# Kernel optimization log

Measured on AMD Instinct MI355X. Metric: run time of the kernel, lower is better.

## Reference

```python
import jax, jax.numpy as jnp
import numpy as np
from jax import lax

OBS_LEN = 8
PRED_LEN = 12
DIM = 128      # hidden_dim
EMB = 64       # embedding_dim
HEADS = 4
MODES = 5
SCENE = 32     # peds per scene
NPED = 8192    # total peds (256 scenes)


def _lin(key, out_d, in_d):
    kw, kb = jax.random.split(key)
    w = jax.random.normal(kw, (out_d, in_d), jnp.float32) / np.sqrt(in_d).astype(np.float32)
    b = jax.random.normal(kb, (out_d,), jnp.float32) * 0.01
    return w, b


def _stack(key, n, out_d, in_d):
    ws, bs = zip(*[_lin(k, out_d, in_d) for k in jax.random.split(key, n)])
    return jnp.stack(ws), jnp.stack(bs)


def setup_inputs() -> dict:
    key = jax.random.key(0)
    ks = jax.random.split(key, 24)
    inp = {}
    inp['obs_traj'] = jax.random.normal(ks[0], (OBS_LEN, NPED, 2), jnp.float32)
    inp['pe_w'], inp['pe_b'] = _lin(ks[1], EMB, 2)
    inp['lstm_wih'], inp['lstm_bih'] = _lin(ks[2], 4 * DIM, EMB)
    inp['lstm_whh'], inp['lstm_bhh'] = _lin(ks[3], 4 * DIM, DIM)
    inp['rp_w1'], inp['rp_b1'] = _lin(ks[4], DIM // 2, 2)
    inp['rp_w2'], inp['rp_b2'] = _lin(ks[5], DIM, DIM // 2)
    inp['wq'], inp['bq'] = _lin(ks[6], DIM, DIM)
    inp['wk'], inp['bk'] = _lin(ks[7], DIM, DIM)
    inp['wv'], inp['bv'] = _lin(ks[8], DIM, DIM)
    inp['wo'], inp['bo'] = _lin(ks[9], DIM, DIM)
    inp['op_w'], inp['op_b'] = _lin(ks[10], DIM, 2 * DIM)
    inp['mp_w1'], inp['mp_b1'] = _lin(ks[11], DIM, 2 * DIM)
    inp['mp_w2'], inp['mp_b2'] = _lin(ks[12], MODES, DIM)
    inp['td_w1'], inp['td_b1'] = _stack(ks[13], MODES, DIM, 2 * DIM)
    inp['td_w2'], inp['td_b2'] = _stack(ks[14], MODES, DIM, DIM)
    inp['td_w3'], inp['td_b3'] = _stack(ks[15], MODES, PRED_LEN * 2, DIM)
    inp['ud_w1'], inp['ud_b1'] = _stack(ks[16], MODES, DIM // 2, 2 * DIM)
    inp['ud_w2'], inp['ud_b2'] = _stack(ks[17], MODES, PRED_LEN * 2, DIM // 2)
    inp['scene_size'] = SCENE
    return inp


def reference(obs_traj, pe_w, pe_b, lstm_wih, lstm_bih, lstm_whh, lstm_bhh,
              rp_w1, rp_b1, rp_w2, rp_b2, wq, bq, wk, bk, wv, bv, wo, bo,
              op_w, op_b, mp_w1, mp_b1, mp_w2, mp_b2,
              td_w1, td_b1, td_w2, td_b2, td_w3, td_b3,
              ud_w1, ud_b1, ud_w2, ud_b2, scene_size):
    obs = jnp.transpose(obs_traj, (1, 0, 2))          # (N, T, 2)
    N = obs.shape[0]
    D = lstm_whh.shape[1]

    # ---- NodeHistoryEncoder: Linear embed + 1-layer LSTM, last hidden ----
    emb = jnp.einsum('ntd,ed->nte', obs, pe_w) + pe_b  # (N, T, EMB)

    def step(carry, x):
        h, c = carry
        g = x @ lstm_wih.T + lstm_bih + h @ lstm_whh.T + lstm_bhh
        i, f, gg, o = jnp.split(g, 4, axis=-1)          # torch gate order i,f,g,o
        c = jax.nn.sigmoid(f) * c + jax.nn.sigmoid(i) * jnp.tanh(gg)
        h = jax.nn.sigmoid(o) * jnp.tanh(c)
        return (h, c), None

    h0 = jnp.zeros((N, D), obs.dtype)
    (node_features, _), _ = lax.scan(step, (h0, h0), jnp.swapaxes(emb, 0, 1))
    last_pos = obs[:, -1, :]                            # (N, 2)

    # ---- EdgeEncoder: per-scene rel-pos-biased multi-head attention ----
    S = scene_size
    B = N // S
    feat = node_features.reshape(B, S, D)
    pos = last_pos.reshape(B, S, 2)
    rel = pos[:, None, :, :] - pos[:, :, None, :]       # [b,i,j] = pos_j - pos_i
    rel_enc = jax.nn.relu(jnp.einsum('bijd,hd->bijh', rel, rp_w1) + rp_b1)
    rel_enc = jnp.einsum('bijh,eh->bije', rel_enc, rp_w2) + rp_b2  # (B,S,S,D)
    kv = feat[:, None, :, :] + rel_enc                  # key == value
    dh = D // HEADS
    q = (feat @ wq.T + bq).reshape(B, S, HEADS, dh)
    kp = (jnp.einsum('bijd,ed->bije', kv, wk) + bk).reshape(B, S, S, HEADS, dh)
    vp = (jnp.einsum('bijd,ed->bije', kv, wv) + bv).reshape(B, S, S, HEADS, dh)
    scores = jnp.einsum('bihd,bijhd->bhij', q, kp) / np.sqrt(dh).astype(np.float32)
    attn = jax.nn.softmax(scores, axis=-1)
    ctx = jnp.einsum('bhij,bijhd->bihd', attn, vp).reshape(B, S, D)
    attn_out = ctx @ wo.T + bo
    edge = (jnp.concatenate([feat, attn_out], axis=-1) @ op_w.T + op_b).reshape(N, D)

    f_all = jnp.concatenate([node_features, edge], axis=-1)  # (N, 2D)

    # ---- GMMDecoder ----
    probs = jax.nn.softmax(jax.nn.relu(f_all @ mp_w1.T + mp_b1) @ mp_w2.T + mp_b2, axis=-1)
    h1 = jax.nn.relu(jnp.einsum('nd,mhd->nmh', f_all, td_w1) + td_b1)    # (N,M,D)
    h2 = jax.nn.relu(jnp.einsum('nmh,mgh->nmg', h1, td_w2) + td_b2)
    traj = (jnp.einsum('nmg,mog->nmo', h2, td_w3) + td_b3).reshape(N, MODES, PRED_LEN, 2)
    u1 = jax.nn.relu(jnp.einsum('nd,mhd->nmh', f_all, ud_w1) + ud_b1)
    sigmas = jax.nn.softplus(jnp.einsum('nmh,moh->nmo', u1, ud_w2) + ud_b2).reshape(N, MODES, PRED_LEN, 2)
    predictions = jnp.cumsum(traj, axis=2) + last_pos[:, None, None, :]
    return predictions, probs
```

## Files before the change

kernel.cpp:

```cpp
#include <hip/hip_runtime.h>
#include <math.h>

typedef __attribute__((ext_vector_type(8))) short short8;
typedef __attribute__((ext_vector_type(4))) float f32x4;

#define NPED 8192
#define INVS 0.1767766952966369f

#define B_WHH    0
#define B_WQKV   131072
#define B_WO     229376
#define B_OPW    262144
#define B_MPW1   327680
#define B_TDW1   393216
#define B_TDW2   720896
#define B_WK2PAD 884736
#define F_WIHE   950272
#define F_BEFF   954368
#define F_WV2T   956416
#define F_BQKV   989184
#define F_ZERO   990720
#define A_FEAT   991744
#define A_QKV    3088896
#define A_H1MP   9380352
#define A_H1TD   11477504
#define A_QW     11477504
#define B_TDW3C  21963264
#define F_TDB3C  22004224

__device__ __forceinline__ float bf2f(ushort u) {
  union { unsigned i; float f; } v; v.i = ((unsigned)u) << 16; return v.f;
}
__device__ __forceinline__ float blo(unsigned u) {
  union { unsigned i; float f; } v; v.i = u << 16; return v.f;
}
__device__ __forceinline__ float bhi(unsigned u) {
  union { unsigned i; float f; } v; v.i = u & 0xffff0000u; return v.f;
}
__device__ __forceinline__ ushort f2bf(float f) {
  union { float f; unsigned i; } v; v.f = f;
  unsigned r = v.i + 0x7fffu + ((v.i >> 16) & 1u);
  return (ushort)(r >> 16);
}

__global__ __launch_bounds__(256) void prep(
    const float* __restrict__ wih, const float* __restrict__ bih, const float* __restrict__ bhh,
    const float* __restrict__ pew, const float* __restrict__ peb,
    const float* __restrict__ wk, const float* __restrict__ wv,
    const float* __restrict__ rpw2, const float* __restrict__ rpb2,
    const float* __restrict__ bq, const float* __restrict__ bk, const float* __restrict__ bv,
    const float* __restrict__ whh, const float* __restrict__ wq, const float* __restrict__ wo,
    const float* __restrict__ opw, const float* __restrict__ mpw1,
    const float* __restrict__ tdw1, const float* __restrict__ tdw2,
    const float* __restrict__ tdw3, const float* __restrict__ tdb3,
    char* __restrict__ wsb) {
  int tid = blockIdx.x * 256 + threadIdx.x;
  float* wihe = (float*)(wsb + F_WIHE);
  float* beff = (float*)(wsb + F_BEFF);
  float* wv2T = (float*)(wsb + F_WV2T);
  float* bqkv = (float*)(wsb + F_BQKV);
  if (tid < 512) {
    int d = tid;
    float s0 = 0.f, s1 = 0.f, sb = 0.f;
    for (int e = 0; e < 64; ++e) {
      float w = wih[d * 64 + e];
      s0 += w * pew[e * 2]; s1 += w * pew[e * 2 + 1]; sb += w * peb[e];
    }
    wihe[d * 2] = s0; wihe[d * 2 + 1] = s1;
    beff[d] = bih[d] + bhh[d] + sb;
  } else if (tid < 33280) {
    int idx = tid - 512; int r = idx >> 7, d = idx & 127;
    int h = r >> 6, e = r & 63;
    float s = 0.f;
    if ((d >> 5) == h)
      for (int c = 0; c < 128; ++c) s += wk[d * 128 + c] * rpw2[c * 64 + e];
    ((ushort*)(wsb + B_WK2PAD))[idx] = f2bf(s);
  } else if (tid < 41472) {
    int idx = tid - 33280; int e = idx >> 7, hd = idx & 127;
    float s = 0.f;
    for (int c = 0; c < 128; ++c) s += wv[hd * 128 + c] * rpw2[c * 64 + e];
    wv2T[idx] = s;
  } else if (tid < 41600) {
    int d = tid - 41472;
    float s = bk[d];
    for (int c = 0; c < 128; ++c) s += wk[d * 128 + c] * rpb2[c];
    bqkv[128 + d] = s;
  } else if (tid < 41728) {
    int d = tid - 41600;
    float s = bv[d];
    for (int c = 0; c < 128; ++c) s += wv[d * 128 + c] * rpb2[c];
    bqkv[256 + d] = s;
  } else if (tid < 41856) {
    int d = tid - 41728;
    bqkv[d] = bq[d] * INVS;
  } else if (tid < 42112) {
    ((float*)(wsb + F_ZERO))[tid - 41856] = 0.f;
  } else {
    int i = tid - 42112;
    if (i < 65536) {
      ((ushort*)(wsb + B_WHH))[i] = f2bf(whh[i]);
    } else if (i < 114688) {
      int j = i - 65536; int n = j >> 7, k = j & 127;
      float v = (n < 128) ? wq[n * 128 + k] * INVS
                          : (n < 256) ? wk[(n - 128) * 128 + k] : wv[(n - 256) * 128 + k];
      ((ushort*)(wsb + B_WQKV))[j] = f2bf(v);
    } else if (i < 131072) {
      int j = i - 114688; ((ushort*)(wsb + B_WO))[j] = f2bf(wo[j]);
    } else if (i < 163840) {
      int j = i - 131072; ((ushort*)(wsb + B_OPW))[j] = f2bf(opw[j]);
    } else if (i < 196608) {
      int j = i - 163840; ((ushort*)(wsb + B_MPW1))[j] = f2bf(mpw1[j]);
    } else if (i < 360448) {
      int j = i - 196608; ((ushort*)(wsb + B_TDW1))[j] = f2bf(tdw1[j]);
    } else if (i < 442368) {
      int j = i - 360448; ((ushort*)(wsb + B_TDW2))[j] = f2bf(tdw2[j]);
    } else if (i < 462848) {
      int j = i - 442368; int m = j >> 12, r = j & 4095, o = r >> 7, k = r & 127;
      float s = 0.f;
      if (o < 24) {
        int c = o & 1, jj = o >> 1;
        for (int jp = 0; jp <= jj; ++jp) s += tdw3[(m * 24 + jp * 2 + c) * 128 + k];
      }
      ((ushort*)(wsb + B_TDW3C))[j] = f2bf(s);
    } else if (i < 462968) {
      int j = i - 462848; int m = j / 24, o = j % 24;
      int c = o & 1, jj = o >> 1;
      float s = 0.f;
      for (int jp = 0; jp <= jj; ++jp) s += tdb3[m * 24 + jp * 2 + c];
      ((float*)(wsb + F_TDB3C))[j] = s;
    }
  }
}

__global__ __launch_bounds__(512) void lstm_mfma(
    const float* __restrict__ obs, const ushort* __restrict__ whhb,
    const float* __restrict__ wihe, const float* __restrict__ beff,
    ushort* __restrict__ feat) {
  __shared__ ushort Hs[32 * 128];
  __shared__ float obs_s[8][32][2];
  int tid = threadIdx.x;
  int w = tid >> 6, l = tid & 63;
  int lm = l & 15, lg = l >> 4;
  int nb = blockIdx.x * 32;
  {
    int ts = tid >> 6, p = (tid >> 1) & 31, c = tid & 1;
    obs_s[ts][p][c] = obs[ts * (NPED * 2) + (nb + p) * 2 + c];
  }
  for (int i = tid; i < 4096; i += 512) Hs[i] = 0;
  short8 bfr[4][4];
  float wx0[4], wx1[4], be[4];
#pragma unroll
  for (int q = 0; q < 4; ++q) {
    int g = q * 128 + w * 16 + lm;
    wx0[q] = wihe[g * 2]; wx1[q] = wihe[g * 2 + 1]; be[q] = beff[g];
#pragma unroll
    for (int ks = 0; ks < 4; ++ks)
      bfr[q][ks] = *(const short8*)(const void*)&whhb[g * 128 + ks * 32 + lg * 8];
  }
  float cst[2][4] = {};
  __syncthreads();
  for (int ts = 0; ts < 8; ++ts) {
    f32x4 acc[2][4];
#pragma unroll
    for (int mi = 0; mi < 2; ++mi)
#pragma unroll
      for (int r = 0; r < 4; ++r) {
        int p = mi * 16 + lg * 4 + r;
        float ox = obs_s[ts][p][0], oy = obs_s[ts][p][1];
#pragma unroll
        for (int q = 0; q < 4; ++q)
          acc[mi][q][r] = be[q] + wx0[q] * ox + wx1[q] * oy;
      }
#pragma unroll
    for (int ks = 0; ks < 4; ++ks) {
      int p0 = lm, p1 = 16 + lm;
      short8 a0 = *(const short8*)(const void*)&Hs[p0 * 128 + ((ks * 32 + lg * 8) ^ ((p0 & 7) << 3))];
      short8 a1 = *(const short8*)(const void*)&Hs[p1 * 128 + ((ks * 32 + lg * 8) ^ ((p1 & 7) << 3))];
#pragma unroll
      for (int q = 0; q < 4; ++q) {
        acc[0][q] = __builtin_amdgcn_mfma_f32_16x16x32_bf16(a0, bfr[q][ks], acc[0][q], 0, 0, 0);
        acc[1][q] = __builtin_amdgcn_mfma_f32_16x16x32_bf16(a1, bfr[q][ks], acc[1][q], 0, 0, 0);
      }
    }
    __syncthreads();
    int d = w * 16 + lm;
#pragma unroll
    for (int mi = 0; mi < 2; ++mi)
#pragma unroll
      for (int r = 0; r < 4; ++r) {
        int p = mi * 16 + lg * 4 + r;
        float xi = acc[mi][0][r], xf = acc[mi][1][r], xg = acc[mi][2][r], xo = acc[mi][3][r];
        float ig = 1.f / (1.f + __expf(-xi));
        float fg = 1.f / (1.f + __expf(-xf));
        xg = fminf(fmaxf(xg, -30.f), 30.f);
        float eg = __expf(-2.f * xg);
        float gg = (1.f - eg) / (1.f + eg);
        float og = 1.f / (1.f + __expf(-xo));
        float cv = fg * cst[mi][r] + ig * gg;
        cst[mi][r] = cv;
        float cvc = fminf(fmaxf(cv, -30.f), 30.f);
        float ec = __expf(-2.f * cvc);
        float th = (1.f - ec) / (1.f + ec);
        ushort hb = f2bf(og * th);
        Hs[p * 128 + (d ^ ((p & 7) << 3))] = hb;
        if (ts == 7) feat[(size_t)(nb + p) * 128 + d] = hb;
      }
    __syncthreads();
  }
}

template<int NF>
__global__ __launch_bounds__(256) void mfma_gemm(
    const ushort* __restrict__ A1, int lda1, int K1,
    const ushort* __restrict__ A2, int lda2,
    const ushort* __restrict__ Bw, int K,
    const float* __restrict__ bias,
    ushort* __restrict__ out, int ldo, int ooff, int relu,
    int sB, int sBias, int sA1, int sOut) {
  int w = threadIdx.x >> 6, l = threadIdx.x & 63;
  int lm = l & 15, lg = l >> 4;
  int z = blockIdx.z;
  A1 += (size_t)z * sA1;
  Bw += (size_t)z * sB;
  bias += (size_t)z * sBias;
  out += (size_t)z * sOut;
  int row = blockIdx.x * 64 + w * 16 + lm;
  int col0 = blockIdx.y * (NF * 16);
  f32x4 acc[NF];
#pragma unroll
  for (int i = 0; i < NF; ++i) acc[i] = (f32x4){0.f, 0.f, 0.f, 0.f};
  const int nks = K >> 5;
  for (int ks = 0; ks < nks; ++ks) {
    int kb = ks * 32 + lg * 8;
    const ushort* ap = (ks * 32 < K1) ? (A1 + (size_t)row * lda1 + kb)
                                      : (A2 + (size_t)row * lda2 + (kb - K1));
    short8 af = *(const short8*)(const void*)ap;
#pragma unroll
    for (int ni = 0; ni < NF; ++ni) {
      short8 bf = *(const short8*)(const void*)(Bw + (size_t)(col0 + ni * 16 + lm) * K + kb);
      acc[ni] = __builtin_amdgcn_mfma_f32_16x16x32_bf16(af, bf, acc[ni], 0, 0, 0);
    }
  }
  int orow0 = blockIdx.x * 64 + w * 16 + lg * 4;
#pragma unroll
  for (int ni = 0; ni < NF; ++ni) {
    int c = col0 + ni * 16 + lm;
    float bv = bias[c];
#pragma unroll
    for (int r = 0; r < 4; ++r) {
      float v = acc[ni][r] + bv;
      if (relu) v = fmaxf(v, 0.f);
      out[(size_t)(orow0 + r) * ldo + ooff + c] = f2bf(v);
    }
  }
}

__global__ __launch_bounds__(256) void traj_mfma(
    const ushort* __restrict__ TD2, const ushort* __restrict__ w3c,
    const float* __restrict__ b3c, const float* __restrict__ obs,
    float* __restrict__ out) {
  int w = threadIdx.x >> 6, l = threadIdx.x & 63;
  int lm = l & 15, lg = l >> 4;
  int m = blockIdx.y;
  const ushort* A = TD2 + (size_t)m * (NPED * 128);
  const ushort* B = w3c + (size_t)m * 4096;
  int row = blockIdx.x * 64 + w * 16 + lm;
  f32x4 acc[2];
  acc[0] = (f32x4){0.f,0.f,0.f,0.f}; acc[1] = (f32x4){0.f,0.f,0.f,0.f};
#pragma unroll
  for (int ks = 0; ks < 4; ++ks) {
    int kb = ks * 32 + lg * 8;
    short8 af = *(const short8*)(const void*)(A + (size_t)row * 128 + kb);
#pragma unroll
    for (int ni = 0; ni < 2; ++ni) {
      short8 bf = *(const short8*)(const void*)(B + (ni * 16 + lm) * 128 + kb);
      acc[ni] = __builtin_amdgcn_mfma_f32_16x16x32_bf16(af, bf, acc[ni], 0, 0, 0);
    }
  }
  int orow0 = blockIdx.x * 64 + w * 16 + lg * 4;
#pragma unroll
  for (int ni = 0; ni < 2; ++ni) {
    int o = ni * 16 + lm;
    if (o < 24) {
      float bb = b3c[m * 24 + o];
      int c = o & 1;
#pragma unroll
      for (int r = 0; r < 4; ++r) {
        int n = orow0 + r;
        out[(size_t)n * 120 + m * 24 + o] = acc[ni][r] + bb + obs[7 * (NPED * 2) + n * 2 + c];
      }
    }
  }
}

__global__ __launch_bounds__(256) void attn_kernel(
    const float* __restrict__ obs, ushort* QKV, const ushort* __restrict__ QW,
    const float* __restrict__ wv2T,
    const float* __restrict__ rpw1, const float* __restrict__ rpb1) {
  __shared__ ushort K0s[32 * 128];
  __shared__ ushort V0s[32 * 128];
  __shared__ ushort renc[4 * 32 * 64];
  __shared__ float Qi[4][128];
  __shared__ float QWs[4][256];
  __shared__ float att[4][4][32];
  __shared__ float AR[4][4][64];
  __shared__ float rpx[64], rpy[64], rpb[64];
  __shared__ float posS[32][2];
  __shared__ float posI[4][2];
  int t = threadIdx.x;
  int scene = blockIdx.x & 255, ic = blockIdx.x >> 8;
  int i0 = ic * 4, sbase = scene * 32;

  for (int idx = t; idx < 1024; idx += 256) {
    int arr = idx >> 9, j = (idx >> 4) & 31, c = idx & 15;
    short8 v = *(const short8*)(const void*)&QKV[(size_t)(sbase + j) * 384 + 128 + arr * 128 + c * 8];
    ushort* dst = arr ? V0s : K0s;
    *(short8*)(void*)&dst[j * 128 + (c ^ (j & 7)) * 8] = v;
  }
  for (int idx = t; idx < 512; idx += 256) {
    int ii = idx >> 7, d = idx & 127;
    Qi[ii][d] = bf2f(QKV[(size_t)(sbase + i0 + ii) * 384 + d]);
  }
  for (int idx = t; idx < 1024; idx += 256) {
    int ii = idx >> 8, e = idx & 255;
    QWs[ii][e] = bf2f(QW[(size_t)(sbase + i0 + ii) * 256 + e]);
  }
  if (t < 64) posS[t >> 1][t & 1] = obs[7 * (NPED * 2) + (sbase + (t >> 1)) * 2 + (t & 1)];
  else if (t < 72) {
    int q = t - 64;
    posI[q >> 1][q & 1] = obs[7 * (NPED * 2) + (sbase + i0 + (q >> 1)) * 2 + (q & 1)];
  } else if (t >= 128 && t < 192) {
    int e = t - 128;
    rpx[e] = rpw1[e * 2]; rpy[e] = rpw1[e * 2 + 1]; rpb[e] = rpb1[e];
  }
  __syncthreads();

  for (int idx = t; idx < 1024; idx += 256) {
    int ii = idx >> 8, j = (idx >> 3) & 31, c = idx & 7;
    float dx = posS[j][0] - posI[ii][0], dy = posS[j][1] - posI[ii][1];
    short8 pk;
#pragma unroll
    for (int r = 0; r < 8; ++r) {
      int e = c * 8 + r;
      pk[r] = (short)f2bf(fmaxf(rpx[e] * dx + rpy[e] * dy + rpb[e], 0.f));
    }
    *(short8*)(void*)&renc[(ii * 32 + j) * 64 + (c ^ (j & 7)) * 8] = pk;
  }
  __syncthreads();

  for (int idx = t; idx < 512; idx += 256) {
    int ii = idx >> 7, h = (idx >> 5) & 3, j = idx & 31;
    float s = 0.f;
#pragma unroll
    for (int cc = 0; cc < 4; ++cc) {
      uint4 kv = *(const uint4*)(const void*)&K0s[j * 128 + (((h * 4 + cc) ^ (j & 7)) * 8)];
      const float4 qa = *(const float4*)&Qi[ii][h * 32 + cc * 8];
      const float4 qb = *(const float4*)&Qi[ii][h * 32 + cc * 8 + 4];
      s += blo(kv.x) * qa.x + bhi(kv.x) * qa.y + blo(kv.y) * qa.z + bhi(kv.y) * qa.w;
      s += blo(kv.z) * qb.x + bhi(kv.z) * qb.y + blo(kv.w) * qb.z + bhi(kv.w) * qb.w;
    }
#pragma unroll
    for (int c = 0; c < 8; ++c) {
      uint4 rv = *(const uint4*)(const void*)&renc[(ii * 32 + j) * 64 + ((c ^ (j & 7)) * 8)];
      const float4 wa = *(const float4*)&QWs[ii][c * 8];
      const float4 wb = *(const float4*)&QWs[ii][c * 8 + 4];
      (void)wa; (void)wb;
      const float4 ua = *(const float4*)&QWs[ii][h * 64 + c * 8];
      const float4 ub = *(const float4*)&QWs[ii][h * 64 + c * 8 + 4];
      s += blo(rv.x) * ua.x + bhi(rv.x) * ua.y + blo(rv.y) * ua.z + bhi(rv.y) * ua.w;
      s += blo(rv.z) * ub.x + bhi(rv.z) * ub.y + blo(rv.w) * ub.z + bhi(rv.w) * ub.w;
    }
    att[ii][h][j] = s;
  }
  __syncthreads();

  {
    int r = t >> 4, lj = t & 15;
    float v0 = att[r >> 2][r & 3][lj], v1 = att[r >> 2][r & 3][lj + 16];
    float mx = fmaxf(v0, v1);
    mx = fmaxf(mx, __shfl_xor(mx, 8, 16));
    mx = fmaxf(mx, __shfl_xor(mx, 4, 16));
    mx = fmaxf(mx, __shfl_xor(mx, 2, 16));
    mx = fmaxf(mx, __shfl_xor(mx, 1, 16));
    float e0 = expf(v0 - mx), e1 = expf(v1 - mx);
    float sm = e0 + e1;
    sm += __shfl_xor(sm, 8, 16);
    sm += __shfl_xor(sm, 4, 16);
    sm += __shfl_xor(sm, 2, 16);
    sm += __shfl_xor(sm, 1, 16);
    float inv = 1.f / sm;
    att[r >> 2][r & 3][lj] = e0 * inv;
    att[r >> 2][r & 3][lj + 16] = e1 * inv;
  }
  __syncthreads();

  {
    int ii = t >> 6, h = (t >> 4) & 3, e4 = t & 15;
    int c = e4 >> 1, off = (e4 & 1) * 4;
    float a0 = 0.f, a1 = 0.f, a2 = 0.f, a3 = 0.f;
    for (int j = 0; j < 32; ++j) {
      float av = att[ii][h][j];
      uint2 rv = *(const uint2*)(const void*)&renc[(ii * 32 + j) * 64 + ((c ^ (j & 7)) * 8) + off];
      a0 += av * blo(rv.x); a1 += av * bhi(rv.x);
      a2 += av * blo(rv.y); a3 += av * bhi(rv.y);
    }
    *(float4*)&AR[ii][h][e4 * 4] = make_float4(a0, a1, a2, a3);
  }
  __syncthreads();

  {
    int ii = t >> 6, l = t & 63;
    int h5 = l >> 5, hd4 = l & 31;
    int hd = hd4 * 4, h = hd >> 5;
    float c0 = 0.f, c1 = 0.f, c2 = 0.f, c3 = 0.f;
    int cch = hd >> 3, offh = hd & 7;
    for (int j = h5 * 16; j < h5 * 16 + 16; ++j) {
      float av = att[ii][h][j];
      uint2 vv = *(const uint2*)(const void*)&V0s[j * 128 + ((cch ^ (j & 7)) * 8) + offh];
      c0 += av * blo(vv.x); c1 += av * bhi(vv.x);
      c2 += av * blo(vv.y); c3 += av * bhi(vv.y);
    }
    for (int e4 = h5 * 8; e4 < h5 * 8 + 8; ++e4) {
      const float4 ar = *(const float4*)&AR[ii][h][e4 * 4];
#pragma unroll
      for (int r = 0; r < 4; ++r) {
        const float4 wv = *(const float4*)&wv2T[(e4 * 4 + r) * 128 + hd];
        float a = (r == 0) ? ar.x : (r == 1) ? ar.y : (r == 2) ? ar.z : ar.w;
        c0 += a * wv.x; c1 += a * wv.y; c2 += a * wv.z; c3 += a * wv.w;
      }
    }
    c0 += __shfl_xor(c0, 32); c1 += __shfl_xor(c1, 32);
    c2 += __shfl_xor(c2, 32); c3 += __shfl_xor(c3, 32);
    if (h5 == 0) {
      ushort4 o;
      o.x = f2bf(c0); o.y = f2bf(c1); o.z = f2bf(c2); o.w = f2bf(c3);
      *(ushort4*)(void*)&QKV[(size_t)(sbase + i0 + ii) * 384 + hd] = o;
    }
  }
}

__global__ __launch_bounds__(256) void probs_kernel(
    const ushort* __restrict__ H1, const float* __restrict__ mpw2,
    const float* __restrict__ mpb2, float* __restrict__ out) {
  __shared__ float Hsm[64][129];
  __shared__ float lgt[64][5];
  int t = threadIdx.x, nb = blockIdx.x * 64;
  for (int idx = t; idx < 8192; idx += 256) Hsm[idx >> 7][idx & 127] = bf2f(H1[(size_t)nb * 128 + idx]);
  __syncthreads();
  for (int idx = t; idx < 320; idx += 256) {
    int p = idx / 5, m = idx % 5;
    float s = mpb2[m];
    for (int k = 0; k < 128; ++k) s += Hsm[p][k] * mpw2[m * 128 + k];
    lgt[p][m] = s;
  }
  __syncthreads();
  if (t < 64) {
    float m0 = lgt[t][0];
#pragma unroll
    for (int j = 1; j < 5; ++j) m0 = fmaxf(m0, lgt[t][j]);
    float e[5], s = 0.f;
#pragma unroll
    for (int j = 0; j < 5; ++j) { e[j] = expf(lgt[t][j] - m0); s += e[j]; }
    float inv = 1.f / s;
#pragma unroll
    for (int j = 0; j < 5; ++j) out[983040 + (size_t)(nb + t) * 5 + j] = e[j] * inv;
  }
}

extern "C" void kernel_launch(void* const* d_in, const int* in_sizes, int n_in,
                              void* d_out, int out_size, void* d_ws, size_t ws_size,
                              hipStream_t stream) {
  (void)in_sizes; (void)n_in; (void)out_size; (void)ws_size;
  const float* obs  = (const float*)d_in[0];
  const float* pew  = (const float*)d_in[1];
  const float* peb  = (const float*)d_in[2];
  const float* wih  = (const float*)d_in[3];
  const float* bih  = (const float*)d_in[4];
  const float* whh  = (const float*)d_in[5];
  const float* bhh  = (const float*)d_in[6];
  const float* rpw1 = (const float*)d_in[7];
  const float* rpb1 = (const float*)d_in[8];
  const float* rpw2 = (const float*)d_in[9];
  const float* rpb2 = (const float*)d_in[10];
  const float* wq   = (const float*)d_in[11];
  const float* bq   = (const float*)d_in[12];
  const float* wk   = (const float*)d_in[13];
  const float* bk   = (const float*)d_in[14];
  const float* wv   = (const float*)d_in[15];
  const float* bv   = (const float*)d_in[16];
  const float* wo   = (const float*)d_in[17];
  const float* bo   = (const float*)d_in[18];
  const float* opw  = (const float*)d_in[19];
  const float* opb  = (const float*)d_in[20];
  const float* mpw1 = (const float*)d_in[21];
  const float* mpb1 = (const float*)d_in[22];
  const float* mpw2 = (const float*)d_in[23];
  const float* mpb2 = (const float*)d_in[24];
  const float* tdw1 = (const float*)d_in[25];
  const float* tdb1 = (const float*)d_in[26];
  const float* tdw2 = (const float*)d_in[27];
  const float* tdb2 = (const float*)d_in[28];
  const float* tdw3 = (const float*)d_in[29];
  const float* tdb3 = (const float*)d_in[30];
  char* wsb = (char*)d_ws;
  float* out = (float*)d_out;

  ushort* whhb   = (ushort*)(wsb + B_WHH);
  ushort* wqkvb  = (ushort*)(wsb + B_WQKV);
  ushort* wob    = (ushort*)(wsb + B_WO);
  ushort* opwb   = (ushort*)(wsb + B_OPW);
  ushort* mpw1b  = (ushort*)(wsb + B_MPW1);
  ushort* tdw1b  = (ushort*)(wsb + B_TDW1);
  ushort* tdw2b  = (ushort*)(wsb + B_TDW2);
  ushort* wk2pb  = (ushort*)(wsb + B_WK2PAD);
  ushort* tdw3cb = (ushort*)(wsb + B_TDW3C);
  ushort* featb  = (ushort*)(wsb + A_FEAT);
  ushort* qkvb   = (ushort*)(wsb + A_QKV);
  ushort* qwb    = (ushort*)(wsb + A_QW);
  ushort* h1mpb  = (ushort*)(wsb + A_H1MP);
  ushort* h1tdb  = (ushort*)(wsb + A_H1TD);

  prep<<<1973, 256, 0, stream>>>(wih, bih, bhh, pew, peb, wk, wv, rpw2, rpb2,
                                 bq, bk, bv, whh, wq, wo, opw, mpw1, tdw1, tdw2,
                                 tdw3, tdb3, wsb);
  lstm_mfma<<<256, 512, 0, stream>>>(obs, whhb, (float*)(wsb + F_WIHE),
                                     (float*)(wsb + F_BEFF), featb);
  mfma_gemm<4><<<dim3(128, 6, 1), 256, 0, stream>>>(
      featb, 128, 128, featb, 128, wqkvb, 128, (float*)(wsb + F_BQKV),
      qkvb, 384, 0, 0, 0, 0, 0, 0);
  mfma_gemm<4><<<dim3(128, 4, 1), 256, 0, stream>>>(
      qkvb, 384, 128, qkvb, 384, wk2pb, 128, (float*)(wsb + F_ZERO),
      qwb, 256, 0, 0, 0, 0, 0, 0);
  attn_kernel<<<2048, 256, 0, stream>>>(obs, qkvb, qwb, (float*)(wsb + F_WV2T), rpw1, rpb1);
  mfma_gemm<4><<<dim3(128, 2, 1), 256, 0, stream>>>(
      qkvb, 384, 128, qkvb, 384, wob, 128, bo, qkvb, 384, 128, 0, 0, 0, 0, 0);
  mfma_gemm<4><<<dim3(128, 2, 1), 256, 0, stream>>>(
      featb, 128, 128, qkvb + 128, 384, opwb, 256, opb, qkvb, 384, 256, 0, 0, 0, 0, 0);
  mfma_gemm<4><<<dim3(128, 2, 1), 256, 0, stream>>>(
      featb, 128, 128, qkvb + 256, 384, mpw1b, 256, mpb1, h1mpb, 128, 0, 1, 0, 0, 0, 0);
  probs_kernel<<<128, 256, 0, stream>>>(h1mpb, mpw2, mpb2, out);
  mfma_gemm<4><<<dim3(128, 2, 5), 256, 0, stream>>>(
      featb, 128, 128, qkvb + 256, 384, tdw1b, 256, tdb1, h1tdb, 128, 0, 1,
      32768, 128, 0, 1048576);
  mfma_gemm<8><<<dim3(128, 1, 5), 256, 0, stream>>>(
      h1tdb, 128, 128, h1tdb, 128, tdw2b, 128, tdb2, h1tdb, 128, 0, 1,
      16384, 128, 1048576, 1048576);
  traj_mfma<<<dim3(128, 5), 256, 0, stream>>>(h1tdb, tdw3cb, (float*)(wsb + F_TDB3C), obs, out);
}
```

Measured before the change: 297.3 us.

## Fold Wo into edge projection and fuse decoder MLP chains into single kernels

Folds the attention output projection (wo, bo) into the op_w edge projection in prep, so one GEMM replaces two. The mode-probability MLP and softmax become a single kernel, and the three trajectory-decoder layers are chained through shared memory in one kernel, so the h1/h2 intermediates no longer round-trip through global memory. The QKV buffer is widened to hold QW and edge outputs, and GEMM sizes become template constants so the k-loop fully unrolls. The trade-offs are heavier per-block register and LDS use, and lower parallelism in the fused decoder kernel.

```diff
diff --git a/kernel.cpp b/kernel.cpp
--- a/kernel.cpp
+++ b/kernel.cpp
@@ -9,24 +9,21 @@
 
 #define B_WHH    0
 #define B_WQKV   131072
-#define B_WO     229376
-#define B_OPW    262144
-#define B_MPW1   327680
-#define B_TDW1   393216
-#define B_TDW2   720896
-#define B_WK2PAD 884736
-#define F_WIHE   950272
-#define F_BEFF   954368
-#define F_WV2T   956416
-#define F_BQKV   989184
-#define F_ZERO   990720
-#define A_FEAT   991744
-#define A_QKV    3088896
-#define A_H1MP   9380352
-#define A_H1TD   11477504
-#define A_QW     11477504
-#define B_TDW3C  21963264
-#define F_TDB3C  22004224
+#define B_WK2PAD 229376
+#define B_OPWE   294912
+#define B_MPW1   360448
+#define B_TDW1   425984
+#define B_TDW2   753664
+#define B_TDW3C  917504
+#define F_WIHE   958464
+#define F_BEFF   962560
+#define F_WV2T   964608
+#define F_BQKV   997376
+#define F_BEDGE  998912
+#define F_TDB3C  999424
+#define F_ZERO   999936
+#define A_FEAT   1000960
+#define A_QKV    3098112
 
 __device__ __forceinline__ float bf2f(ushort u) {
   union { unsigned i; float f; } v; v.i = ((unsigned)u) << 16; return v.f;
@@ -50,15 +47,12 @@
     const float* __restrict__ rpw2, const float* __restrict__ rpb2,
     const float* __restrict__ bq, const float* __restrict__ bk, const float* __restrict__ bv,
     const float* __restrict__ whh, const float* __restrict__ wq, const float* __restrict__ wo,
-    const float* __restrict__ opw, const float* __restrict__ mpw1,
+    const float* __restrict__ opw, const float* __restrict__ opb, const float* __restrict__ bo,
+    const float* __restrict__ mpw1,
     const float* __restrict__ tdw1, const float* __restrict__ tdw2,
     const float* __restrict__ tdw3, const float* __restrict__ tdb3,
     char* __restrict__ wsb) {
   int tid = blockIdx.x * 256 + threadIdx.x;
-  float* wihe = (float*)(wsb + F_WIHE);
-  float* beff = (float*)(wsb + F_BEFF);
-  float* wv2T = (float*)(wsb + F_WV2T);
-  float* bqkv = (float*)(wsb + F_BQKV);
   if (tid < 512) {
     int d = tid;
     float s0 = 0.f, s1 = 0.f, sb = 0.f;
@@ -66,69 +60,77 @@
       float w = wih[d * 64 + e];
       s0 += w * pew[e * 2]; s1 += w * pew[e * 2 + 1]; sb += w * peb[e];
     }
-    wihe[d * 2] = s0; wihe[d * 2 + 1] = s1;
-    beff[d] = bih[d] + bhh[d] + sb;
-  } else if (tid < 33280) {
-    int idx = tid - 512; int r = idx >> 7, d = idx & 127;
+    ((float*)(wsb + F_WIHE))[d * 2] = s0;
+    ((float*)(wsb + F_WIHE))[d * 2 + 1] = s1;
+    ((float*)(wsb + F_BEFF))[d] = bih[d] + bhh[d] + sb;
+  } else if (tid < 49664) {
+    int j = tid - 512; int n = j >> 7, k = j & 127;
+    float v = (n < 128) ? wq[n * 128 + k] * INVS
+                        : (n < 256) ? wk[(n - 128) * 128 + k] : wv[(n - 256) * 128 + k];
+    ((ushort*)(wsb + B_WQKV))[j] = f2bf(v);
+  } else if (tid < 82432) {
+    int idx = tid - 49664; int r = idx >> 7, d = idx & 127;
     int h = r >> 6, e = r & 63;
     float s = 0.f;
     if ((d >> 5) == h)
       for (int c = 0; c < 128; ++c) s += wk[d * 128 + c] * rpw2[c * 64 + e];
     ((ushort*)(wsb + B_WK2PAD))[idx] = f2bf(s);
-  } else if (tid < 41472) {
-    int idx = tid - 33280; int e = idx >> 7, hd = idx & 127;
+  } else if (tid < 115200) {
+    int idx = tid - 82432; int o = idx >> 8, k = idx & 255;
+    float s;
+    if (k < 128) s = opw[o * 256 + k];
+    else {
+      s = 0.f;
+      for (int c = 0; c < 128; ++c) s += opw[o * 256 + 128 + c] * wo[c * 128 + (k - 128)];
+    }
+    ((ushort*)(wsb + B_OPWE))[idx] = f2bf(s);
+  } else if (tid < 147968) {
+    int j = tid - 115200; ((ushort*)(wsb + B_MPW1))[j] = f2bf(mpw1[j]);
+  } else if (tid < 311808) {
+    int j = tid - 147968; ((ushort*)(wsb + B_TDW1))[j] = f2bf(tdw1[j]);
+  } else if (tid < 393728) {
+    int j = tid - 311808; ((ushort*)(wsb + B_TDW2))[j] = f2bf(tdw2[j]);
+  } else if (tid < 414208) {
+    int j = tid - 393728; int m = j >> 12, r = j & 4095, o = r >> 7, k = r & 127;
+    float s = 0.f;
+    if (o < 24) {
+      int c = o & 1, jj = o >> 1;
+      for (int jp = 0; jp <= jj; ++jp) s += tdw3[(m * 24 + jp * 2 + c) * 128 + k];
+    }
+    ((ushort*)(wsb + B_TDW3C))[j] = f2bf(s);
+  } else if (tid < 414328) {
+    int j = tid - 414208; int m = j / 24, o = j % 24;
+    int c = o & 1, jj = o >> 1;
+    float s = 0.f;
+    for (int jp = 0; jp <= jj; ++jp) s += tdb3[m * 24 + jp * 2 + c];
+    ((float*)(wsb + F_TDB3C))[j] = s;
+  } else if (tid < 414712) {
+    int d = tid - 414328;
+    float s;
+    if (d < 128) s = bq[d] * INVS;
+    else if (d < 256) {
+      int dd = d - 128; s = bk[dd];
+      for (int c = 0; c < 128; ++c) s += wk[dd * 128 + c] * rpb2[c];
+    } else {
+      int dd = d - 256; s = bv[dd];
+      for (int c = 0; c < 128; ++c) s += wv[dd * 128 + c] * rpb2[c];
+    }
+    ((float*)(wsb + F_BQKV))[d] = s;
+  } else if (tid < 414840) {
+    int o = tid - 414712;
+    float s = opb[o];
+    for (int c = 0; c < 128; ++c) s += opw[o * 256 + 128 + c] * bo[c];
+    ((float*)(wsb + F_BEDGE))[o] = s;
+  } else if (tid < 415096) {
+    ((float*)(wsb + F_ZERO))[tid - 414840] = 0.f;
+  } else if (tid < 423288) {
+    int idx = tid - 415096; int e = idx >> 7, hd = idx & 127;
     float s = 0.f;
     for (int c = 0; c < 128; ++c) s += wv[hd * 128 + c] * rpw2[c * 64 + e];
-    wv2T[idx] = s;
-  } else if (tid < 41600) {
-    int d = tid - 41472;
-    float s = bk[d];
-    for (int c = 0; c < 128; ++c) s += wk[d * 128 + c] * rpb2[c];
-    bqkv[128 + d] = s;
-  } else if (tid < 41728) {
-    int d = tid - 41600;
-    float s = bv[d];
-    for (int c = 0; c < 128; ++c) s += wv[d * 128 + c] * rpb2[c];
-    bqkv[256 + d] = s;
-  } else if (tid < 41856) {
-    int d = tid - 41728;
-    bqkv[d] = bq[d] * INVS;
-  } else if (tid < 42112) {
-    ((float*)(wsb + F_ZERO))[tid - 41856] = 0.f;
-  } else {
-    int i = tid - 42112;
-    if (i < 65536) {
-      ((ushort*)(wsb + B_WHH))[i] = f2bf(whh[i]);
-    } else if (i < 114688) {
-      int j = i - 65536; int n = j >> 7, k = j & 127;
-      float v = (n < 128) ? wq[n * 128 + k] * INVS
-                          : (n < 256) ? wk[(n - 128) * 128 + k] : wv[(n - 256) * 128 + k];
-      ((ushort*)(wsb + B_WQKV))[j] = f2bf(v);
-    } else if (i < 131072) {
-      int j = i - 114688; ((ushort*)(wsb + B_WO))[j] = f2bf(wo[j]);
-    } else if (i < 163840) {
-      int j = i - 131072; ((ushort*)(wsb + B_OPW))[j] = f2bf(opw[j]);
-    } else if (i < 196608) {
-      int j = i - 163840; ((ushort*)(wsb + B_MPW1))[j] = f2bf(mpw1[j]);
-    } else if (i < 360448) {
-      int j = i - 196608; ((ushort*)(wsb + B_TDW1))[j] = f2bf(tdw1[j]);
-    } else if (i < 442368) {
-      int j = i - 360448; ((ushort*)(wsb + B_TDW2))[j] = f2bf(tdw2[j]);
-    } else if (i < 462848) {
-      int j = i - 442368; int m = j >> 12, r = j & 4095, o = r >> 7, k = r & 127;
-      float s = 0.f;
-      if (o < 24) {
-        int c = o & 1, jj = o >> 1;
-        for (int jp = 0; jp <= jj; ++jp) s += tdw3[(m * 24 + jp * 2 + c) * 128 + k];
-      }
-      ((ushort*)(wsb + B_TDW3C))[j] = f2bf(s);
-    } else if (i < 462968) {
-      int j = i - 462848; int m = j / 24, o = j % 24;
-      int c = o & 1, jj = o >> 1;
-      float s = 0.f;
-      for (int jp = 0; jp <= jj; ++jp) s += tdb3[m * 24 + jp * 2 + c];
-      ((float*)(wsb + F_TDB3C))[j] = s;
-    }
+    ((float*)(wsb + F_WV2T))[idx] = s;
+  } else if (tid < 488824) {
+    int i = tid - 423288;
+    ((ushort*)(wsb + B_WHH))[i] = f2bf(whh[i]);
   }
 }
 
@@ -209,35 +211,29 @@
   }
 }
 
-template<int NF>
+template<int NF, int NKS, int K1KS>
 __global__ __launch_bounds__(256) void mfma_gemm(
-    const ushort* __restrict__ A1, int lda1, int K1,
+    const ushort* __restrict__ A1, int lda1,
     const ushort* __restrict__ A2, int lda2,
-    const ushort* __restrict__ Bw, int K,
+    const ushort* __restrict__ Bw,
     const float* __restrict__ bias,
-    ushort* __restrict__ out, int ldo, int ooff, int relu,
-    int sB, int sBias, int sA1, int sOut) {
+    ushort* __restrict__ out, int ldo, int ooff, int relu) {
   int w = threadIdx.x >> 6, l = threadIdx.x & 63;
   int lm = l & 15, lg = l >> 4;
-  int z = blockIdx.z;
-  A1 += (size_t)z * sA1;
-  Bw += (size_t)z * sB;
-  bias += (size_t)z * sBias;
-  out += (size_t)z * sOut;
   int row = blockIdx.x * 64 + w * 16 + lm;
   int col0 = blockIdx.y * (NF * 16);
   f32x4 acc[NF];
 #pragma unroll
   for (int i = 0; i < NF; ++i) acc[i] = (f32x4){0.f, 0.f, 0.f, 0.f};
-  const int nks = K >> 5;
-  for (int ks = 0; ks < nks; ++ks) {
+#pragma unroll
+  for (int ks = 0; ks < NKS; ++ks) {
     int kb = ks * 32 + lg * 8;
-    const ushort* ap = (ks * 32 < K1) ? (A1 + (size_t)row * lda1 + kb)
-                                      : (A2 + (size_t)row * lda2 + (kb - K1));
+    const ushort* ap = (ks < K1KS) ? (A1 + (size_t)row * lda1 + kb)
+                                   : (A2 + (size_t)row * lda2 + (kb - K1KS * 32));
     short8 af = *(const short8*)(const void*)ap;
 #pragma unroll
     for (int ni = 0; ni < NF; ++ni) {
-      short8 bf = *(const short8*)(const void*)(Bw + (size_t)(col0 + ni * 16 + lm) * K + kb);
+      short8 bf = *(const short8*)(const void*)(Bw + (size_t)(col0 + ni * 16 + lm) * (NKS * 32) + kb);
       acc[ni] = __builtin_amdgcn_mfma_f32_16x16x32_bf16(af, bf, acc[ni], 0, 0, 0);
     }
   }
@@ -255,29 +251,148 @@
   }
 }
 
-__global__ __launch_bounds__(256) void traj_mfma(
-    const ushort* __restrict__ TD2, const ushort* __restrict__ w3c,
-    const float* __restrict__ b3c, const float* __restrict__ obs,
+__global__ __launch_bounds__(256) void mp_probs(
+    const ushort* __restrict__ feat, const ushort* __restrict__ qkv,
+    const ushort* __restrict__ w1b, const float* __restrict__ mpb1,
+    const float* __restrict__ mpw2, const float* __restrict__ mpb2,
     float* __restrict__ out) {
-  int w = threadIdx.x >> 6, l = threadIdx.x & 63;
-  int lm = l & 15, lg = l >> 4;
+  __shared__ float w2s[5][128];
+  int t = threadIdx.x;
+  for (int i = t; i < 640; i += 256) w2s[i >> 7][i & 127] = mpw2[i];
+  __syncthreads();
+  int w = t >> 6, l = t & 63, lm = l & 15, lg = l >> 4;
+  int row = blockIdx.x * 64 + w * 16 + lm;
+  f32x4 acc[8];
+#pragma unroll
+  for (int i = 0; i < 8; ++i) acc[i] = (f32x4){0.f, 0.f, 0.f, 0.f};
+#pragma unroll
+  for (int ks = 0; ks < 8; ++ks) {
+    int kb = ks * 32 + lg * 8;
+    const ushort* ap = (ks < 4) ? (feat + (size_t)row * 128 + kb)
+                                : (qkv + (size_t)row * 640 + 256 + (kb - 128));
+    short8 af = *(const short8*)(const void*)ap;
+#pragma unroll
+    for (int ni = 0; ni < 8; ++ni) {
+      short8 bf = *(const short8*)(const void*)(w1b + (size_t)(ni * 16 + lm) * 256 + kb);
+      acc[ni] = __builtin_amdgcn_mfma_f32_16x16x32_bf16(af, bf, acc[ni], 0, 0, 0);
+    }
+  }
+  float bc[8];
+#pragma unroll
+  for (int ni = 0; ni < 8; ++ni) bc[ni] = mpb1[ni * 16 + lm];
+  float lgt[4][5];
+#pragma unroll
+  for (int r = 0; r < 4; ++r)
+#pragma unroll
+    for (int m = 0; m < 5; ++m) {
+      float s = 0.f;
+#pragma unroll
+      for (int ni = 0; ni < 8; ++ni)
+        s += fmaxf(acc[ni][r] + bc[ni], 0.f) * w2s[m][ni * 16 + lm];
+      lgt[r][m] = s;
+    }
+#pragma unroll
+  for (int mask = 1; mask < 16; mask <<= 1)
+#pragma unroll
+    for (int r = 0; r < 4; ++r)
+#pragma unroll
+      for (int m = 0; m < 5; ++m)
+        lgt[r][m] += __shfl_xor(lgt[r][m], mask);
+  if (lm < 5) {
+#pragma unroll
+    for (int r = 0; r < 4; ++r) {
+      float b0 = lgt[r][0] + mpb2[0];
+      float mx = b0;
+      float lv[5]; lv[0] = b0;
+#pragma unroll
+      for (int m = 1; m < 5; ++m) { lv[m] = lgt[r][m] + mpb2[m]; mx = fmaxf(mx, lv[m]); }
+      float sm = 0.f;
+#pragma unroll
+      for (int m = 0; m < 5; ++m) { lv[m] = expf(lv[m] - mx); sm += lv[m]; }
+      int n = blockIdx.x * 64 + w * 16 + lg * 4 + r;
+      out[983040 + (size_t)n * 5 + lm] = lv[lm] / sm;
+    }
+  }
+}
+
+__global__ __launch_bounds__(256) void td_fused(
+    const ushort* __restrict__ feat, const ushort* __restrict__ qkv,
+    const ushort* __restrict__ w1b, const float* __restrict__ tdb1,
+    const ushort* __restrict__ w2b, const float* __restrict__ tdb2,
+    const ushort* __restrict__ w3c, const float* __restrict__ b3c,
+    const float* __restrict__ obs, float* __restrict__ out) {
+  __shared__ ushort slab[64 * 136];
+  int t = threadIdx.x, w = t >> 6, l = t & 63, lm = l & 15, lg = l >> 4;
   int m = blockIdx.y;
-  const ushort* A = TD2 + (size_t)m * (NPED * 128);
-  const ushort* B = w3c + (size_t)m * 4096;
   int row = blockIdx.x * 64 + w * 16 + lm;
-  f32x4 acc[2];
-  acc[0] = (f32x4){0.f,0.f,0.f,0.f}; acc[1] = (f32x4){0.f,0.f,0.f,0.f};
+  const ushort* W1 = w1b + (size_t)m * 32768;
+  const ushort* W2 = w2b + (size_t)m * 16384;
+  const ushort* W3 = w3c + (size_t)m * 4096;
+  const float* B1 = tdb1 + m * 128;
+  const float* B2 = tdb2 + m * 128;
+  f32x4 a1[8];
+#pragma unroll
+  for (int i = 0; i < 8; ++i) a1[i] = (f32x4){0.f, 0.f, 0.f, 0.f};
+#pragma unroll
+  for (int ks = 0; ks < 8; ++ks) {
+    int kb = ks * 32 + lg * 8;
+    const ushort* ap = (ks < 4) ? (feat + (size_t)row * 128 + kb)
+                                : (qkv + (size_t)row * 640 + 256 + (kb - 128));
+    short8 af = *(const short8*)(const void*)ap;
+#pragma unroll
+    for (int ni = 0; ni < 8; ++ni) {
+      short8 bf = *(const short8*)(const void*)(W1 + (size_t)(ni * 16 + lm) * 256 + kb);
+      a1[ni] = __builtin_amdgcn_mfma_f32_16x16x32_bf16(af, bf, a1[ni], 0, 0, 0);
+    }
+  }
+#pragma unroll
+  for (int ni = 0; ni < 8; ++ni) {
+    float bb = B1[ni * 16 + lm];
+#pragma unroll
+    for (int r = 0; r < 4; ++r)
+      slab[(w * 16 + lg * 4 + r) * 136 + ni * 16 + lm] = f2bf(fmaxf(a1[ni][r] + bb, 0.f));
+  }
+  __syncthreads();
+  short8 af2[4];
+#pragma unroll
+  for (int ks = 0; ks < 4; ++ks)
+    af2[ks] = *(const short8*)(const void*)&slab[(w * 16 + lm) * 136 + ks * 32 + lg * 8];
+  f32x4 a2[8];
+#pragma unroll
+  for (int i = 0; i < 8; ++i) a2[i] = (f32x4){0.f, 0.f, 0.f, 0.f};
 #pragma unroll
   for (int ks = 0; ks < 4; ++ks) {
     int kb = ks * 32 + lg * 8;
-    short8 af = *(const short8*)(const void*)(A + (size_t)row * 128 + kb);
+#pragma unroll
+    for (int ni = 0; ni < 8; ++ni) {
+      short8 bf = *(const short8*)(const void*)(W2 + (size_t)(ni * 16 + lm) * 128 + kb);
+      a2[ni] = __builtin_amdgcn_mfma_f32_16x16x32_bf16(af2[ks], bf, a2[ni], 0, 0, 0);
+    }
+  }
+  __syncthreads();
+#pragma unroll
+  for (int ni = 0; ni < 8; ++ni) {
+    float bb = B2[ni * 16 + lm];
+#pragma unroll
+    for (int r = 0; r < 4; ++r)
+      slab[(w * 16 + lg * 4 + r) * 136 + ni * 16 + lm] = f2bf(fmaxf(a2[ni][r] + bb, 0.f));
+  }
+  __syncthreads();
+  short8 af3[4];
+#pragma unroll
+  for (int ks = 0; ks < 4; ++ks)
+    af3[ks] = *(const short8*)(const void*)&slab[(w * 16 + lm) * 136 + ks * 32 + lg * 8];
+  f32x4 a3[2];
+  a3[0] = (f32x4){0.f, 0.f, 0.f, 0.f}; a3[1] = (f32x4){0.f, 0.f, 0.f, 0.f};
+#pragma unroll
+  for (int ks = 0; ks < 4; ++ks) {
+    int kb = ks * 32 + lg * 8;
 #pragma unroll
     for (int ni = 0; ni < 2; ++ni) {
-      short8 bf = *(const short8*)(const void*)(B + (ni * 16 + lm) * 128 + kb);
-      acc[ni] = __builtin_amdgcn_mfma_f32_16x16x32_bf16(af, bf, acc[ni], 0, 0, 0);
-    }
-  }
-  int orow0 = blockIdx.x * 64 + w * 16 + lg * 4;
+      short8 bf = *(const short8*)(const void*)(W3 + (size_t)(ni * 16 + lm) * 128 + kb);
+      a3[ni] = __builtin_amdgcn_mfma_f32_16x16x32_bf16(af3[ks], bf, a3[ni], 0, 0, 0);
+    }
+  }
 #pragma unroll
   for (int ni = 0; ni < 2; ++ni) {
     int o = ni * 16 + lm;
@@ -286,15 +401,15 @@
       int c = o & 1;
 #pragma unroll
       for (int r = 0; r < 4; ++r) {
-        int n = orow0 + r;
-        out[(size_t)n * 120 + m * 24 + o] = acc[ni][r] + bb + obs[7 * (NPED * 2) + n * 2 + c];
+        int n = blockIdx.x * 64 + w * 16 + lg * 4 + r;
+        out[(size_t)n * 120 + m * 24 + o] = a3[ni][r] + bb + obs[7 * (NPED * 2) + n * 2 + c];
       }
     }
   }
 }
 
 __global__ __launch_bounds__(256) void attn_kernel(
-    const float* __restrict__ obs, ushort* QKV, const ushort* __restrict__ QW,
+    const float* __restrict__ obs, ushort* QKV,
     const float* __restrict__ wv2T,
     const float* __restrict__ rpw1, const float* __restrict__ rpb1) {
   __shared__ ushort K0s[32 * 128];
@@ -313,17 +428,17 @@
 
   for (int idx = t; idx < 1024; idx += 256) {
     int arr = idx >> 9, j = (idx >> 4) & 31, c = idx & 15;
-    short8 v = *(const short8*)(const void*)&QKV[(size_t)(sbase + j) * 384 + 128 + arr * 128 + c * 8];
+    short8 v = *(const short8*)(const void*)&QKV[(size_t)(sbase + j) * 640 + 128 + arr * 128 + c * 8];
     ushort* dst = arr ? V0s : K0s;
     *(short8*)(void*)&dst[j * 128 + (c ^ (j & 7)) * 8] = v;
   }
   for (int idx = t; idx < 512; idx += 256) {
     int ii = idx >> 7, d = idx & 127;
-    Qi[ii][d] = bf2f(QKV[(size_t)(sbase + i0 + ii) * 384 + d]);
+    Qi[ii][d] = bf2f(QKV[(size_t)(sbase + i0 + ii) * 640 + d]);
   }
   for (int idx = t; idx < 1024; idx += 256) {
     int ii = idx >> 8, e = idx & 255;
-    QWs[ii][e] = bf2f(QW[(size_t)(sbase + i0 + ii) * 256 + e]);
+    QWs[ii][e] = bf2f(QKV[(size_t)(sbase + i0 + ii) * 640 + 384 + e]);
   }
   if (t < 64) posS[t >> 1][t & 1] = obs[7 * (NPED * 2) + (sbase + (t >> 1)) * 2 + (t & 1)];
   else if (t < 72) {
@@ -362,9 +477,6 @@
 #pragma unroll
     for (int c = 0; c < 8; ++c) {
       uint4 rv = *(const uint4*)(const void*)&renc[(ii * 32 + j) * 64 + ((c ^ (j & 7)) * 8)];
-      const float4 wa = *(const float4*)&QWs[ii][c * 8];
-      const float4 wb = *(const float4*)&QWs[ii][c * 8 + 4];
-      (void)wa; (void)wb;
       const float4 ua = *(const float4*)&QWs[ii][h * 64 + c * 8];
       const float4 ub = *(const float4*)&QWs[ii][h * 64 + c * 8 + 4];
       s += blo(rv.x) * ua.x + bhi(rv.x) * ua.y + blo(rv.y) * ua.z + bhi(rv.y) * ua.w;
@@ -434,36 +546,8 @@
     if (h5 == 0) {
       ushort4 o;
       o.x = f2bf(c0); o.y = f2bf(c1); o.z = f2bf(c2); o.w = f2bf(c3);
-      *(ushort4*)(void*)&QKV[(size_t)(sbase + i0 + ii) * 384 + hd] = o;
-    }
-  }
-}
-
-__global__ __launch_bounds__(256) void probs_kernel(
-    const ushort* __restrict__ H1, const float* __restrict__ mpw2,
-    const float* __restrict__ mpb2, float* __restrict__ out) {
-  __shared__ float Hsm[64][129];
-  __shared__ float lgt[64][5];
-  int t = threadIdx.x, nb = blockIdx.x * 64;
-  for (int idx = t; idx < 8192; idx += 256) Hsm[idx >> 7][idx & 127] = bf2f(H1[(size_t)nb * 128 + idx]);
-  __syncthreads();
-  for (int idx = t; idx < 320; idx += 256) {
-    int p = idx / 5, m = idx % 5;
-    float s = mpb2[m];
-    for (int k = 0; k < 128; ++k) s += Hsm[p][k] * mpw2[m * 128 + k];
-    lgt[p][m] = s;
-  }
-  __syncthreads();
-  if (t < 64) {
-    float m0 = lgt[t][0];
-#pragma unroll
-    for (int j = 1; j < 5; ++j) m0 = fmaxf(m0, lgt[t][j]);
-    float e[5], s = 0.f;
-#pragma unroll
-    for (int j = 0; j < 5; ++j) { e[j] = expf(lgt[t][j] - m0); s += e[j]; }
-    float inv = 1.f / s;
-#pragma unroll
-    for (int j = 0; j < 5; ++j) out[983040 + (size_t)(nb + t) * 5 + j] = e[j] * inv;
+      *(ushort4*)(void*)&QKV[(size_t)(sbase + i0 + ii) * 640 + hd] = o;
+    }
   }
 }
 
@@ -507,43 +591,28 @@
 
   ushort* whhb   = (ushort*)(wsb + B_WHH);
   ushort* wqkvb  = (ushort*)(wsb + B_WQKV);
-  ushort* wob    = (ushort*)(wsb + B_WO);
-  ushort* opwb   = (ushort*)(wsb + B_OPW);
+  ushort* wk2pb  = (ushort*)(wsb + B_WK2PAD);
+  ushort* opweb  = (ushort*)(wsb + B_OPWE);
   ushort* mpw1b  = (ushort*)(wsb + B_MPW1);
   ushort* tdw1b  = (ushort*)(wsb + B_TDW1);
   ushort* tdw2b  = (ushort*)(wsb + B_TDW2);
-  ushort* wk2pb  = (ushort*)(wsb + B_WK2PAD);
   ushort* tdw3cb = (ushort*)(wsb + B_TDW3C);
   ushort* featb  = (ushort*)(wsb + A_FEAT);
   ushort* qkvb   = (ushort*)(wsb + A_QKV);
-  ushort* qwb    = (ushort*)(wsb + A_QW);
-  ushort* h1mpb  = (ushort*)(wsb + A_H1MP);
-  ushort* h1tdb  = (ushort*)(wsb + A_H1TD);
-
-  prep<<<1973, 256, 0, stream>>>(wih, bih, bhh, pew, peb, wk, wv, rpw2, rpb2,
-                                 bq, bk, bv, whh, wq, wo, opw, mpw1, tdw1, tdw2,
-                                 tdw3, tdb3, wsb);
+
+  prep<<<1910, 256, 0, stream>>>(wih, bih, bhh, pew, peb, wk, wv, rpw2, rpb2,
+                                 bq, bk, bv, whh, wq, wo, opw, opb, bo, mpw1,
+                                 tdw1, tdw2, tdw3, tdb3, wsb);
   lstm_mfma<<<256, 512, 0, stream>>>(obs, whhb, (float*)(wsb + F_WIHE),
                                      (float*)(wsb + F_BEFF), featb);
-  mfma_gemm<4><<<dim3(128, 6, 1), 256, 0, stream>>>(
-      featb, 128, 128, featb, 128, wqkvb, 128, (float*)(wsb + F_BQKV),
-      qkvb, 384, 0, 0, 0, 0, 0, 0);
-  mfma_gemm<4><<<dim3(128, 4, 1), 256, 0, stream>>>(
-      qkvb, 384, 128, qkvb, 384, wk2pb, 128, (float*)(wsb + F_ZERO),
-      qwb, 256, 0, 0, 0, 0, 0, 0);
-  attn_kernel<<<2048, 256, 0, stream>>>(obs, qkvb, qwb, (float*)(wsb + F_WV2T), rpw1, rpb1);
-  mfma_gemm<4><<<dim3(128, 2, 1), 256, 0, stream>>>(
-      qkvb, 384, 128, qkvb, 384, wob, 128, bo, qkvb, 384, 128, 0, 0, 0, 0, 0);
-  mfma_gemm<4><<<dim3(128, 2, 1), 256, 0, stream>>>(
-      featb, 128, 128, qkvb + 128, 384, opwb, 256, opb, qkvb, 384, 256, 0, 0, 0, 0, 0);
-  mfma_gemm<4><<<dim3(128, 2, 1), 256, 0, stream>>>(
-      featb, 128, 128, qkvb + 256, 384, mpw1b, 256, mpb1, h1mpb, 128, 0, 1, 0, 0, 0, 0);
-  probs_kernel<<<128, 256, 0, stream>>>(h1mpb, mpw2, mpb2, out);
-  mfma_gemm<4><<<dim3(128, 2, 5), 256, 0, stream>>>(
-      featb, 128, 128, qkvb + 256, 384, tdw1b, 256, tdb1, h1tdb, 128, 0, 1,
-      32768, 128, 0, 1048576);
-  mfma_gemm<8><<<dim3(128, 1, 5), 256, 0, stream>>>(
-      h1tdb, 128, 128, h1tdb, 128, tdw2b, 128, tdb2, h1tdb, 128, 0, 1,
-      16384, 128, 1048576, 1048576);
-  traj_mfma<<<dim3(128, 5), 256, 0, stream>>>(h1tdb, tdw3cb, (float*)(wsb + F_TDB3C), obs, out);
-}
+  mfma_gemm<4, 4, 4><<<dim3(128, 6), 256, 0, stream>>>(
+      featb, 128, featb, 128, wqkvb, (float*)(wsb + F_BQKV), qkvb, 640, 0, 0);
+  mfma_gemm<4, 4, 4><<<dim3(128, 4), 256, 0, stream>>>(
+      qkvb, 640, qkvb, 640, wk2pb, (float*)(wsb + F_ZERO), qkvb, 640, 384, 0);
+  attn_kernel<<<2048, 256, 0, stream>>>(obs, qkvb, (float*)(wsb + F_WV2T), rpw1, rpb1);
+  mfma_gemm<4, 8, 4><<<dim3(128, 2), 256, 0, stream>>>(
+      featb, 128, qkvb, 640, opweb, (float*)(wsb + F_BEDGE), qkvb, 640, 256, 0);
+  mp_probs<<<128, 256, 0, stream>>>(featb, qkvb, mpw1b, mpb1, mpw2, mpb2, out);
+  td_fused<<<dim3(128, 5), 256, 0, stream>>>(featb, qkvb, tdw1b, tdb1, tdw2b, tdb2,
+                                             tdw3cb, (float*)(wsb + F_TDB3C), obs, out);
+}
```

Measured after the change: 276.4 us. -7.0%, faster.
